# Kernel optimization log

Measured on AMD Instinct MI355X. Metric: run time of the kernel, lower is better.

## Reference

```python
import jax, jax.numpy as jnp
import numpy as np

B, C, H, W, HEADS = 8, 256, 64, 64, 4
EPS = 1e-5  # torch InstanceNorm2d default eps


def conv1x1(x, w):
    # w: [out_c, in_c]; x: [b, in_c, h, w]
    return jnp.einsum('oc,bchw->bohw', w, x)


def maxpool2(x):
    b, c, h, w = x.shape
    return x.reshape(b, c, h // 2, 2, w // 2, 2).max(axis=(3, 5))


def inorm_affine(x, g, b):
    # InstanceNorm2d(affine=True): normalize per (batch, channel) over H,W
    m = jnp.mean(x, axis=(2, 3), keepdims=True)
    v = jnp.mean((x - m) ** 2, axis=(2, 3), keepdims=True)
    return (x - m) * jax.lax.rsqrt(v + EPS) * g[None, :, None, None] + b[None, :, None, None]


def setup_inputs() -> dict:
    key = jax.random.key(0)
    ks = jax.random.split(key, 12)
    s = 1.0 / np.sqrt(C)  # fan-in style scaling for 1x1 conv weights
    return {
        'x': jax.random.normal(ks[0], (B, C, H, W), jnp.float32),
        'theta_w': jax.random.normal(ks[1], (C, C), jnp.float32) * s,
        'phi_w': jax.random.normal(ks[2], (C, C), jnp.float32) * s,
        'g_w': jax.random.normal(ks[3], (C // 2, C), jnp.float32) * s,
        'o_w': jax.random.normal(ks[4], (C, C // 2), jnp.float32) * np.sqrt(2.0 / C),
        'nt_w': 1.0 + 0.1 * jax.random.normal(ks[5], (C,), jnp.float32),
        'nt_b': 0.1 * jax.random.normal(ks[6], (C,), jnp.float32),
        'np_w': 1.0 + 0.1 * jax.random.normal(ks[7], (C,), jnp.float32),
        'np_b': 0.1 * jax.random.normal(ks[8], (C,), jnp.float32),
        'ng_w': 1.0 + 0.1 * jax.random.normal(ks[9], (C // 2,), jnp.float32),
        'ng_b': 0.1 * jax.random.normal(ks[10], (C // 2,), jnp.float32),
        'gamma': jnp.float32(0.5),
    }


def reference(x, theta_w, phi_w, g_w, o_w, nt_w, nt_b, np_w, np_b, ng_w, ng_b, gamma):
    b, c, h, w = x.shape
    n = h * w            # query length
    m = n // 4           # key/value length after 2x2 maxpool
    theta = inorm_affine(conv1x1(x, theta_w), nt_w, nt_b)
    phi = inorm_affine(maxpool2(conv1x1(x, phi_w)), np_w, np_b)
    g = inorm_affine(maxpool2(conv1x1(x, g_w)), ng_w, ng_b)
    # custom head layout: channel dim split as (C//heads, heads), head dim INNER
    theta_ = theta.reshape(b, c // HEADS, HEADS, n)
    phi_ = phi.reshape(b, c // HEADS, HEADS, m)
    g_ = g.reshape(b, (c // 2) // HEADS, HEADS, m)
    beta = jax.nn.softmax(jnp.einsum('bchi,bchj->bhij', theta_, phi_), axis=-1)
    o = jnp.einsum('bchj,bhij->bchi', g_, beta).reshape(b, c // 2, h, w)
    o = conv1x1(o, o_w)
    return gamma * o + x
```

## Files before the change

kernel.cpp:

```cpp
#include <hip/hip_runtime.h>
#include <hip/hip_bf16.h>
#include <math.h>

typedef float f32x4 __attribute__((ext_vector_type(4)));
typedef float f32x16 __attribute__((ext_vector_type(16)));
typedef __bf16 b16x8 __attribute__((ext_vector_type(8)));
typedef __bf16 b16x4 __attribute__((ext_vector_type(4)));
typedef unsigned int u32x2 __attribute__((ext_vector_type(2)));
typedef unsigned int u32x4 __attribute__((ext_vector_type(4)));

#define L2E 1.44269504088896340736f

__global__ void prep_weights(const float* tw, const float* pw, const float* gw,
                             const float* ow, __bf16* Wp, __bf16* OWp) {
    int idx = blockIdx.x * 256 + threadIdx.x;
    if (idx < 640 * 256) {
        int m = idx >> 8, k = idx & 255;
        float v;
        if (m < 256)      { int o = ((m & 63) << 2) + (m >> 6);            v = tw[o * 256 + k]; }
        else if (m < 512) { int mm = m - 256; int o = ((mm & 63) << 2) + (mm >> 6); v = pw[o * 256 + k]; }
        else              { int mm = m - 512; int o = ((mm & 31) << 2) + (mm >> 5); v = gw[o * 256 + k]; }
        Wp[idx] = (__bf16)v;
    } else {
        int j = idx - 640 * 256;
        if (j < 256 * 128) {
            int m = j >> 7, c = j & 127;
            int o = ((c & 31) << 2) + (c >> 5);
            OWp[j] = (__bf16)ow[m * 128 + o];
        }
    }
}

__global__ void transpose_x(const float* x, __bf16* xt) {
    __shared__ float tile[32][33];
    int b = blockIdx.z, c0 = blockIdx.y * 32, p0 = blockIdx.x * 32;
    int tx = threadIdx.x & 31, ty = threadIdx.x >> 5;
#pragma unroll
    for (int i = 0; i < 4; i++) {
        int cy = ty + i * 8;
        tile[cy][tx] = x[((size_t)(b * 256 + c0 + cy)) * 4096 + p0 + tx];
    }
    __syncthreads();
#pragma unroll
    for (int i = 0; i < 4; i++) {
        int py = ty + i * 8;
        xt[((size_t)b * 4096 + p0 + py) * 256 + c0 + tx] = (__bf16)tile[tx][py];
    }
}

__global__ __launch_bounds__(256) void conv_gemm(const __bf16* __restrict__ Wp,
                                                 const __bf16* __restrict__ xt,
                                                 __bf16* theta_t, __bf16* phi_t, __bf16* g_t) {
    int b = blockIdx.z, mt = blockIdx.y, nt = blockIdx.x;
    __shared__ __bf16 Al[128 * 40];
    __shared__ __bf16 Bl[128 * 40];
    int tid = threadIdx.x, l = tid & 63, w = tid >> 6;
    int wm = w >> 1, wn = w & 1, lr = l & 15, lg = l >> 4;
    f32x4 acc[4][4];
#pragma unroll
    for (int i = 0; i < 4; i++)
#pragma unroll
        for (int j = 0; j < 4; j++)
#pragma unroll
            for (int r = 0; r < 4; r++) acc[i][j][r] = 0.f;
    const __bf16* Ag = Wp + (size_t)mt * 128 * 256;
    const __bf16* Bg = xt + ((size_t)b * 4096 + nt * 128) * 256;
    int srow = tid >> 2, scol = (tid & 3) * 8;
    for (int k0 = 0; k0 < 256; k0 += 32) {
        __syncthreads();
#pragma unroll
        for (int hh = 0; hh < 2; hh++) {
            int r = srow + hh * 64;
            *(b16x8*)&Al[r * 40 + scol] = *(const b16x8*)&Ag[(size_t)r * 256 + k0 + scol];
            *(b16x8*)&Bl[r * 40 + scol] = *(const b16x8*)&Bg[(size_t)r * 256 + k0 + scol];
        }
        __syncthreads();
        int ko = lg * 8;
        b16x8 af[4], bfr[4];
#pragma unroll
        for (int i = 0; i < 4; i++) af[i]  = *(b16x8*)&Al[(wm * 64 + i * 16 + lr) * 40 + ko];
#pragma unroll
        for (int i = 0; i < 4; i++) bfr[i] = *(b16x8*)&Bl[(wn * 64 + i * 16 + lr) * 40 + ko];
#pragma unroll
        for (int i = 0; i < 4; i++)
#pragma unroll
            for (int j = 0; j < 4; j++)
                acc[i][j] = __builtin_amdgcn_mfma_f32_16x16x32_bf16(af[i], bfr[j], acc[i][j], 0, 0, 0);
    }
    int rbase = lg * 4;
#pragma unroll
    for (int i = 0; i < 4; i++) {
        int m = mt * 128 + wm * 64 + i * 16 + rbase;
#pragma unroll
        for (int j = 0; j < 4; j++) {
            int p = nt * 128 + wn * 64 + j * 16 + lr;
            b16x4 v;
#pragma unroll
            for (int r = 0; r < 4; r++) v[r] = (__bf16)acc[i][j][r];
            if (m < 256)      *(b16x4*)&theta_t[((size_t)b * 4096 + p) * 256 + m] = v;
            else if (m < 512) *(b16x4*)&phi_t[((size_t)b * 4096 + p) * 256 + (m - 256)] = v;
            else              *(b16x4*)&g_t[((size_t)b * 4096 + p) * 128 + (m - 512)] = v;
        }
    }
}

__global__ void theta_stats(const __bf16* __restrict__ src, float* s1, float* s2) {
    int b = blockIdx.y, rc = blockIdx.x, c = threadIdx.x;
    float a1 = 0.f, a2 = 0.f;
    for (int r = 0; r < 64; r++) {
        float v = (float)src[((size_t)b * 4096 + rc * 64 + r) * 256 + c];
        a1 += v; a2 += v * v;
    }
    atomicAdd(&s1[b * 256 + c], a1);
    atomicAdd(&s2[b * 256 + c], a2);
}

__global__ void pool_phi(const __bf16* __restrict__ src, __bf16* dst, float* s1, float* s2) {
    int b = blockIdx.y, qc = blockIdx.x, c = threadIdx.x;
    float a1 = 0.f, a2 = 0.f;
    for (int qq = 0; qq < 32; qq++) {
        int q = qc * 32 + qq, qy = q >> 5, qx = q & 31;
        size_t base = ((size_t)(b * 4096) + qy * 128 + qx * 2) * 256 + c;
        float v0 = (float)src[base], v1 = (float)src[base + 256];
        float v2 = (float)src[base + 16384], v3 = (float)src[base + 16640];
        float m = fmaxf(fmaxf(v0, v1), fmaxf(v2, v3));
        dst[((size_t)b * 1024 + q) * 256 + c] = (__bf16)m;
        a1 += m; a2 += m * m;
    }
    atomicAdd(&s1[b * 256 + c], a1);
    atomicAdd(&s2[b * 256 + c], a2);
}

__global__ __launch_bounds__(256) void pool_gT(const __bf16* __restrict__ src, __bf16* gT,
                                               float* s1, float* s2) {
    __shared__ __bf16 Pt[64][136];
    int b = blockIdx.y, qc = blockIdx.x;
    int t = threadIdx.x, c = t & 127, qh = t >> 7;
    float a1 = 0.f, a2 = 0.f;
    for (int qq = 0; qq < 32; qq++) {
        int ql = qh * 32 + qq, q = qc * 64 + ql;
        int qy = q >> 5, qx = q & 31;
        size_t base = ((size_t)(b * 4096) + qy * 128 + qx * 2) * 128 + c;
        float v0 = (float)src[base], v1 = (float)src[base + 128];
        float v2 = (float)src[base + 8192], v3 = (float)src[base + 8320];
        float m = fmaxf(fmaxf(v0, v1), fmaxf(v2, v3));
        Pt[ql][c] = (__bf16)m;
        a1 += m; a2 += m * m;
    }
    atomicAdd(&s1[b * 128 + c], a1);
    atomicAdd(&s2[b * 128 + c], a2);
    __syncthreads();
    int hh = c >> 5, ch = c & 31;
#pragma unroll
    for (int sg = 0; sg < 4; sg++) {
        int seg = qh * 4 + sg;
        b16x8 v;
#pragma unroll
        for (int e = 0; e < 8; e++) v[e] = Pt[seg * 8 + e][c];
        *(b16x8*)&gT[((((size_t)(b * 4 + hh) * 16 + qc) * 8 + seg) * 32 + ch) * 8] = v;
    }
}

__global__ void finalize_stats(const float* s1t, const float* s2t, const float* s1p,
                               const float* s2p, const float* s1g, const float* s2g,
                               const float* ntw, const float* ntb, const float* npw,
                               const float* npb, const float* ngw, const float* ngb,
                               float* sct, float* bit, float* scp, float* bip,
                               float* scg, float* big) {
    int idx = blockIdx.x * 256 + threadIdx.x;
    if (idx >= 8 * 640) return;
    int b = idx / 640, c = idx % 640;
    if (c < 256) {
        float n = 4096.f;
        float m = s1t[b * 256 + c] / n, v = s2t[b * 256 + c] / n - m * m;
        float r = rsqrtf(v + 1e-5f);
        int o = ((c & 63) << 2) + (c >> 6);
        float wv = ntw[o], bv = ntb[o];
        sct[b * 256 + c] = r * wv * L2E;
        bit[b * 256 + c] = (bv - m * r * wv) * L2E;
    } else if (c < 512) {
        int cc = c - 256;
        float n = 1024.f;
        float m = s1p[b * 256 + cc] / n, v = s2p[b * 256 + cc] / n - m * m;
        float r = rsqrtf(v + 1e-5f);
        int o = ((cc & 63) << 2) + (cc >> 6);
        float wv = npw[o], bv = npb[o];
        scp[b * 256 + cc] = r * wv; bip[b * 256 + cc] = bv - m * r * wv;
    } else {
        int cc = c - 512;
        float n = 1024.f;
        float m = s1g[b * 128 + cc] / n, v = s2g[b * 128 + cc] / n - m * m;
        float r = rsqrtf(v + 1e-5f);
        int o = ((cc & 31) << 2) + (cc >> 5);
        float wv = ngw[o], bv = ngb[o];
        scg[b * 128 + cc] = r * wv; big[b * 128 + cc] = bv - m * r * wv;
    }
}

__global__ void normalize_kv(__bf16* phi, __bf16* gT, const float* scp, const float* bip,
                             const float* scg, const float* big) {
    int blk = blockIdx.x, t = threadIdx.x;
    if (blk < 1024) {
        int b = blk >> 7, xi = (blk & 127) * 256 + t;
        int row = xi >> 5, c = (xi & 31) * 8;
        size_t off = ((size_t)b * 1024 + row) * 256 + c;
        b16x8 v = *(b16x8*)&phi[off];
#pragma unroll
        for (int e = 0; e < 8; e++)
            v[e] = (__bf16)((float)v[e] * scp[b * 256 + c + e] + bip[b * 256 + c + e]);
        *(b16x8*)&phi[off] = v;
    } else {
        int f = (blk - 1024) * 256 + t;
        int ch = f & 31, bh = f >> 12;
        int b = bh >> 2;
        int ci = b * 128 + ((bh & 3) << 5) + ch;
        float sc = scg[ci], bi = big[ci];
        size_t off = (size_t)f * 8;
        b16x8 v = *(b16x8*)&gT[off];
#pragma unroll
        for (int e = 0; e < 8; e++) v[e] = (__bf16)((float)v[e] * sc + bi);
        *(b16x8*)&gT[off] = v;
    }
}

__global__ __launch_bounds__(256, 2) void attn(const __bf16* __restrict__ theta_t,
                                               const __bf16* __restrict__ phi_n,
                                               const __bf16* __restrict__ gTz,
                                               const float* __restrict__ sct,
                                               const float* __restrict__ bit,
                                               __bf16* __restrict__ o_mid) {
    int qt = blockIdx.x, h = blockIdx.y, b = blockIdx.z;
    __shared__ __bf16 Kl[2][64 * 64];
    int tid = threadIdx.x, w = tid >> 6, lane = tid & 63;
    int l31 = lane & 31, hi = lane >> 5;
    int qb = qt * 256 + w * 64;

    b16x8 qf[2][4];
#pragma unroll
    for (int m = 0; m < 2; m++) {
        int q = qb + m * 32 + l31;
        const __bf16* qp = theta_t + ((size_t)b * 4096 + q) * 256 + h * 64;
#pragma unroll
        for (int st = 0; st < 4; st++) {
            int cb = st * 16 + hi * 8;
            b16x8 raw = *(const b16x8*)&qp[cb];
            b16x8 nv;
#pragma unroll
            for (int e = 0; e < 8; e++) {
                int cix = b * 256 + h * 64 + cb + e;
                nv[e] = (__bf16)((float)raw[e] * sct[cix] + bit[cix]);
            }
            qf[m][st] = nv;
        }
    }

    const __bf16* Kg = phi_n + (size_t)b * 1024 * 256 + h * 64;
    const __bf16* Vg = gTz + (size_t)(b * 4 + h) * 32768;

    int r0 = tid >> 3, sl = tid & 7, r1 = r0 + 32;
    int gcol = sl * 8;
    int w0 = (sl ^ (r0 & 7)) * 8;
    int w1 = (sl ^ (r1 & 7)) * 8;

    {
        b16x8 k0 = *(const b16x8*)&Kg[(size_t)r0 * 256 + gcol];
        b16x8 k1 = *(const b16x8*)&Kg[(size_t)r1 * 256 + gcol];
        *(b16x8*)&Kl[0][r0 * 64 + w0] = k0;
        *(b16x8*)&Kl[0][r1 * 64 + w1] = k1;
    }
    b16x8 av[4];
#pragma unroll
    for (int js = 0; js < 4; js++)
        av[js] = *(const b16x8*)&Vg[(size_t)(((js * 2 + hi) * 32 + l31) * 8)];
    __syncthreads();

    f32x16 NEG24;
#pragma unroll
    for (int r = 0; r < 16; r++) NEG24[r] = -24.f;
    f32x16 oacc[2];
#pragma unroll
    for (int m = 0; m < 2; m++)
#pragma unroll
        for (int r = 0; r < 16; r++) oacc[m][r] = 0.f;
    float l_run[2] = {0.f, 0.f};

    for (int c = 0; c < 16; c++) {
        int cur = c & 1;
        b16x8 kr0, kr1, avn[4];
        if (c < 15) {
            size_t cb = (size_t)(c + 1) * 64;
            kr0 = *(const b16x8*)&Kg[(cb + r0) * 256 + gcol];
            kr1 = *(const b16x8*)&Kg[(cb + r1) * 256 + gcol];
#pragma unroll
            for (int js = 0; js < 4; js++)
                avn[js] = *(const b16x8*)&Vg[(size_t)((((c + 1) * 8 + js * 2 + hi) * 32 + l31) * 8)];
        }
        b16x8 ak[2][4];
#pragma unroll
        for (int kf = 0; kf < 2; kf++)
#pragma unroll
            for (int st = 0; st < 4; st++)
                ak[kf][st] = *(b16x8*)&Kl[cur][(kf * 32 + l31) * 64 + ((st * 2 + hi) ^ (l31 & 7)) * 8];

#pragma unroll
        for (int m = 0; m < 2; m++) {
            f32x16 s[2];
#pragma unroll
            for (int kf = 0; kf < 2; kf++) {
                s[kf] = __builtin_amdgcn_mfma_f32_32x32x16_bf16(ak[kf][0], qf[m][0], NEG24, 0, 0, 0);
#pragma unroll
                for (int st = 1; st < 4; st++)
                    s[kf] = __builtin_amdgcn_mfma_f32_32x32x16_bf16(ak[kf][st], qf[m][st], s[kf], 0, 0, 0);
            }
            float sum = 0.f;
#pragma unroll
            for (int kf = 0; kf < 2; kf++)
#pragma unroll
                for (int r = 0; r < 16; r++) {
                    float p = __builtin_amdgcn_exp2f(s[kf][r]);
                    s[kf][r] = p; sum += p;
                }
            l_run[m] += sum;
#pragma unroll
            for (int kf = 0; kf < 2; kf++)
#pragma unroll
                for (int hh2 = 0; hh2 < 2; hh2++) {
                    b16x4 A4, B4;
#pragma unroll
                    for (int e = 0; e < 4; e++) {
                        A4[e] = (__bf16)s[kf][hh2 * 8 + e];
                        B4[e] = (__bf16)s[kf][hh2 * 8 + 4 + e];
                    }
                    u32x2 a2 = __builtin_bit_cast(u32x2, A4);
                    u32x2 b2 = __builtin_bit_cast(u32x2, B4);
                    u32x2 q0 = __builtin_amdgcn_permlane32_swap(a2[0], b2[0], false, false);
                    u32x2 q1 = __builtin_amdgcn_permlane32_swap(a2[1], b2[1], false, false);
                    u32x4 pd = {q0[0], q1[0], q0[1], q1[1]};
                    b16x8 pf = __builtin_bit_cast(b16x8, pd);
                    oacc[m] = __builtin_amdgcn_mfma_f32_32x32x16_bf16(av[kf * 2 + hh2], pf, oacc[m], 0, 0, 0);
                }
        }
        if (c < 15) {
            *(b16x8*)&Kl[cur ^ 1][r0 * 64 + w0] = kr0;
            *(b16x8*)&Kl[cur ^ 1][r1 * 64 + w1] = kr1;
            __syncthreads();
#pragma unroll
            for (int js = 0; js < 4; js++) av[js] = avn[js];
        }
    }
#pragma unroll
    for (int m = 0; m < 2; m++) {
        float lr = l_run[m] + __shfl_xor(l_run[m], 32, 64);
        float rl = 1.0f / lr;
        int q = qb + m * 32 + l31;
#pragma unroll
        for (int rr = 0; rr < 4; rr++) {
            b16x4 v;
#pragma unroll
            for (int e = 0; e < 4; e++) v[e] = (__bf16)(oacc[m][rr * 4 + e] * rl);
            *(b16x4*)&o_mid[((size_t)b * 4096 + q) * 128 + h * 32 + rr * 8 + hi * 4] = v;
        }
    }
}

__global__ __launch_bounds__(256) void out_gemm(const __bf16* __restrict__ OWp,
                                                const __bf16* __restrict__ o_mid,
                                                const float* __restrict__ x,
                                                const float* gamma, float* out) {
    int b = blockIdx.z, mt = blockIdx.y, nt = blockIdx.x;
    __shared__ __bf16 Al[128 * 40];
    __shared__ __bf16 Bl[128 * 40];
    int tid = threadIdx.x, l = tid & 63, w = tid >> 6;
    int wm = w >> 1, wn = w & 1, lr = l & 15, lg = l >> 4;
    f32x4 acc[4][4];
#pragma unroll
    for (int i = 0; i < 4; i++)
#pragma unroll
        for (int j = 0; j < 4; j++)
#pragma unroll
            for (int r = 0; r < 4; r++) acc[i][j][r] = 0.f;
    const __bf16* Ag = OWp + (size_t)mt * 128 * 128;
    const __bf16* Bg = o_mid + ((size_t)b * 4096 + nt * 128) * 128;
    int srow = tid >> 2, scol = (tid & 3) * 8;
    for (int k0 = 0; k0 < 128; k0 += 32) {
        __syncthreads();
#pragma unroll
        for (int hh = 0; hh < 2; hh++) {
            int r = srow + hh * 64;
            *(b16x8*)&Al[r * 40 + scol] = *(const b16x8*)&Ag[(size_t)r * 128 + k0 + scol];
            *(b16x8*)&Bl[r * 40 + scol] = *(const b16x8*)&Bg[(size_t)r * 128 + k0 + scol];
        }
        __syncthreads();
        int ko = lg * 8;
        b16x8 af[4], bfr[4];
#pragma unroll
        for (int i = 0; i < 4; i++) af[i]  = *(b16x8*)&Al[(wm * 64 + i * 16 + lr) * 40 + ko];
#pragma unroll
        for (int i = 0; i < 4; i++) bfr[i] = *(b16x8*)&Bl[(wn * 64 + i * 16 + lr) * 40 + ko];
#pragma unroll
        for (int i = 0; i < 4; i++)
#pragma unroll
            for (int j = 0; j < 4; j++)
                acc[i][j] = __builtin_amdgcn_mfma_f32_16x16x32_bf16(af[i], bfr[j], acc[i][j], 0, 0, 0);
    }
    float gm = gamma[0];
    int rbase = lg * 4;
#pragma unroll
    for (int i = 0; i < 4; i++) {
        int m = mt * 128 + wm * 64 + i * 16 + rbase;
#pragma unroll
        for (int j = 0; j < 4; j++) {
            int p = nt * 128 + wn * 64 + j * 16 + lr;
#pragma unroll
            for (int r = 0; r < 4; r++) {
                size_t o = ((size_t)b * 256 + m + r) * 4096 + p;
                out[o] = gm * acc[i][j][r] + x[o];
            }
        }
    }
}

extern "C" void kernel_launch(void* const* d_in, const int* in_sizes, int n_in,
                              void* d_out, int out_size, void* d_ws, size_t ws_size,
                              hipStream_t stream) {
    const float* x   = (const float*)d_in[0];
    const float* tw  = (const float*)d_in[1];
    const float* pw  = (const float*)d_in[2];
    const float* gw  = (const float*)d_in[3];
    const float* ow  = (const float*)d_in[4];
    const float* ntw = (const float*)d_in[5];
    const float* ntb = (const float*)d_in[6];
    const float* npw = (const float*)d_in[7];
    const float* npb = (const float*)d_in[8];
    const float* ngw = (const float*)d_in[9];
    const float* ngb = (const float*)d_in[10];
    const float* gamma = (const float*)d_in[11];
    float* out = (float*)d_out;
    char* ws = (char*)d_ws;

    __bf16* Wp  = (__bf16*)(ws + 0);
    __bf16* OWp = (__bf16*)(ws + 327680);
    __bf16* xt  = (__bf16*)(ws + 393216);
    __bf16* th  = (__bf16*)(ws + 17170432);
    __bf16* phr = (__bf16*)(ws + 33947648);
    __bf16* ghr = (__bf16*)(ws + 50724864);
    __bf16* php = (__bf16*)(ws + 59113472);
    __bf16* gT  = (__bf16*)(ws + 63307776);
    float* sums = (float*)(ws + 65404928);
    float* sb   = (float*)(ws + 65445888);
    __bf16* om  = xt;

    float *s1t = sums, *s2t = sums + 2048, *s1p = sums + 4096, *s2p = sums + 6144,
          *s1g = sums + 8192, *s2g = sums + 9216;
    float *sct = sb, *bit = sb + 2048, *scp = sb + 4096, *bip = sb + 6144,
          *scg = sb + 8192, *big = sb + 9216;

    hipMemsetAsync(sums, 0, 40960, stream);
    prep_weights<<<768, 256, 0, stream>>>(tw, pw, gw, ow, Wp, OWp);
    transpose_x<<<dim3(128, 8, 8), 256, 0, stream>>>(x, xt);
    conv_gemm<<<dim3(32, 5, 8), 256, 0, stream>>>(Wp, xt, th, phr, ghr);
    theta_stats<<<dim3(64, 8), 256, 0, stream>>>(th, s1t, s2t);
    pool_phi<<<dim3(32, 8), 256, 0, stream>>>(phr, php, s1p, s2p);
    pool_gT<<<dim3(16, 8), 256, 0, stream>>>(ghr, gT, s1g, s2g);
    finalize_stats<<<20, 256, 0, stream>>>(s1t, s2t, s1p, s2p, s1g, s2g,
                                           ntw, ntb, npw, npb, ngw, ngb,
                                           sct, bit, scp, bip, scg, big);
    normalize_kv<<<1536, 256, 0, stream>>>(php, gT, scp, bip, scg, big);
    attn<<<dim3(16, 4, 8), 256, 0, stream>>>(th, php, gT, sct, bit, om);
    out_gemm<<<dim3(32, 2, 8), 256, 0, stream>>>(OWp, om, x, gamma, out);
}
```

Before: 126.2 us.

## Pre-layout K into MFMA fragment order, drop LDS staging, fold g-norm into epilogue

The phi normalization now writes K in a per-(batch,head) fragment-major layout, so attention can load K and V straight from global memory into registers with a two-stage register double buffer. This removes the shared-memory K tile and its barriers. The affine norm of g is applied after the softmax-weighted sum, which is valid because the softmax rows sum to one, so g no longer needs a normalize pass. The block index is remapped so blocks sharing a batch-head are spread across the grid, and the atomics plus memset for the statistics are replaced by per-chunk partial sums reduced in finalize_stats. In exchange there is more register pressure, K/V are read repeatedly from L2 instead of LDS, and the score init changes from -24 to 0, which could overflow exp2 for large logits.

```diff
diff --git a/kernel.cpp b/kernel.cpp
--- a/kernel.cpp
+++ b/kernel.cpp
@@ -104,18 +104,18 @@
     }
 }
 
-__global__ void theta_stats(const __bf16* __restrict__ src, float* s1, float* s2) {
+__global__ void theta_stats(const __bf16* __restrict__ src, float* p1, float* p2) {
     int b = blockIdx.y, rc = blockIdx.x, c = threadIdx.x;
     float a1 = 0.f, a2 = 0.f;
-    for (int r = 0; r < 64; r++) {
-        float v = (float)src[((size_t)b * 4096 + rc * 64 + r) * 256 + c];
+    for (int r = 0; r < 256; r++) {
+        float v = (float)src[((size_t)b * 4096 + rc * 256 + r) * 256 + c];
         a1 += v; a2 += v * v;
     }
-    atomicAdd(&s1[b * 256 + c], a1);
-    atomicAdd(&s2[b * 256 + c], a2);
-}
-
-__global__ void pool_phi(const __bf16* __restrict__ src, __bf16* dst, float* s1, float* s2) {
+    p1[(b * 16 + rc) * 256 + c] = a1;
+    p2[(b * 16 + rc) * 256 + c] = a2;
+}
+
+__global__ void pool_phi(const __bf16* __restrict__ src, __bf16* dst, float* p1, float* p2) {
     int b = blockIdx.y, qc = blockIdx.x, c = threadIdx.x;
     float a1 = 0.f, a2 = 0.f;
     for (int qq = 0; qq < 32; qq++) {
@@ -127,12 +127,12 @@
         dst[((size_t)b * 1024 + q) * 256 + c] = (__bf16)m;
         a1 += m; a2 += m * m;
     }
-    atomicAdd(&s1[b * 256 + c], a1);
-    atomicAdd(&s2[b * 256 + c], a2);
+    p1[(b * 32 + qc) * 256 + c] = a1;
+    p2[(b * 32 + qc) * 256 + c] = a2;
 }
 
 __global__ __launch_bounds__(256) void pool_gT(const __bf16* __restrict__ src, __bf16* gT,
-                                               float* s1, float* s2) {
+                                               float* p1, float* p2) {
     __shared__ __bf16 Pt[64][136];
     int b = blockIdx.y, qc = blockIdx.x;
     int t = threadIdx.x, c = t & 127, qh = t >> 7;
@@ -147,8 +147,8 @@
         Pt[ql][c] = (__bf16)m;
         a1 += m; a2 += m * m;
     }
-    atomicAdd(&s1[b * 128 + c], a1);
-    atomicAdd(&s2[b * 128 + c], a2);
+    p1[(b * 16 + qc) * 256 + t] = a1;
+    p2[(b * 16 + qc) * 256 + t] = a2;
     __syncthreads();
     int hh = c >> 5, ch = c & 31;
 #pragma unroll
@@ -161,8 +161,8 @@
     }
 }
 
-__global__ void finalize_stats(const float* s1t, const float* s2t, const float* s1p,
-                               const float* s2p, const float* s1g, const float* s2g,
+__global__ void finalize_stats(const float* tp1, const float* tp2, const float* pp1,
+                               const float* pp2, const float* gp1, const float* gp2,
                                const float* ntw, const float* ntb, const float* npw,
                                const float* npb, const float* ngw, const float* ngb,
                                float* sct, float* bit, float* scp, float* bip,
@@ -171,8 +171,10 @@
     if (idx >= 8 * 640) return;
     int b = idx / 640, c = idx % 640;
     if (c < 256) {
+        float s1 = 0.f, s2 = 0.f;
+        for (int i = 0; i < 16; i++) { s1 += tp1[(b * 16 + i) * 256 + c]; s2 += tp2[(b * 16 + i) * 256 + c]; }
         float n = 4096.f;
-        float m = s1t[b * 256 + c] / n, v = s2t[b * 256 + c] / n - m * m;
+        float m = s1 / n, v = s2 / n - m * m;
         float r = rsqrtf(v + 1e-5f);
         int o = ((c & 63) << 2) + (c >> 6);
         float wv = ntw[o], bv = ntb[o];
@@ -180,16 +182,23 @@
         bit[b * 256 + c] = (bv - m * r * wv) * L2E;
     } else if (c < 512) {
         int cc = c - 256;
+        float s1 = 0.f, s2 = 0.f;
+        for (int i = 0; i < 32; i++) { s1 += pp1[(b * 32 + i) * 256 + cc]; s2 += pp2[(b * 32 + i) * 256 + cc]; }
         float n = 1024.f;
-        float m = s1p[b * 256 + cc] / n, v = s2p[b * 256 + cc] / n - m * m;
+        float m = s1 / n, v = s2 / n - m * m;
         float r = rsqrtf(v + 1e-5f);
         int o = ((cc & 63) << 2) + (cc >> 6);
         float wv = npw[o], bv = npb[o];
         scp[b * 256 + cc] = r * wv; bip[b * 256 + cc] = bv - m * r * wv;
     } else {
         int cc = c - 512;
+        float s1 = 0.f, s2 = 0.f;
+        for (int i = 0; i < 16; i++) {
+            s1 += gp1[(b * 16 + i) * 256 + cc] + gp1[(b * 16 + i) * 256 + 128 + cc];
+            s2 += gp2[(b * 16 + i) * 256 + cc] + gp2[(b * 16 + i) * 256 + 128 + cc];
+        }
         float n = 1024.f;
-        float m = s1g[b * 128 + cc] / n, v = s2g[b * 128 + cc] / n - m * m;
+        float m = s1 / n, v = s2 / n - m * m;
         float r = rsqrtf(v + 1e-5f);
         int o = ((cc & 31) << 2) + (cc >> 5);
         float wv = ngw[o], bv = ngb[o];
@@ -197,40 +206,37 @@
     }
 }
 
-__global__ void normalize_kv(__bf16* phi, __bf16* gT, const float* scp, const float* bip,
-                             const float* scg, const float* big) {
+__global__ void normalize_phi(const __bf16* __restrict__ php, __bf16* __restrict__ phk,
+                              const float* __restrict__ scp, const float* __restrict__ bip) {
     int blk = blockIdx.x, t = threadIdx.x;
-    if (blk < 1024) {
-        int b = blk >> 7, xi = (blk & 127) * 256 + t;
-        int row = xi >> 5, c = (xi & 31) * 8;
-        size_t off = ((size_t)b * 1024 + row) * 256 + c;
-        b16x8 v = *(b16x8*)&phi[off];
+    int b = blk >> 6, h = (blk >> 4) & 3, cc = blk & 15;
+#pragma unroll
+    for (int uu = 0; uu < 2; uu++) {
+        int u = uu * 256 + t;
+        int slot = u >> 6, key = u & 63;
+        int q = cc * 64 + key;
+        int cfull = h * 64 + (slot >> 1) * 16 + (slot & 1) * 8;
+        b16x8 v = *(const b16x8*)&php[((size_t)b * 1024 + q) * 256 + cfull];
+        b16x8 nv;
 #pragma unroll
         for (int e = 0; e < 8; e++)
-            v[e] = (__bf16)((float)v[e] * scp[b * 256 + c + e] + bip[b * 256 + c + e]);
-        *(b16x8*)&phi[off] = v;
-    } else {
-        int f = (blk - 1024) * 256 + t;
-        int ch = f & 31, bh = f >> 12;
-        int b = bh >> 2;
-        int ci = b * 128 + ((bh & 3) << 5) + ch;
-        float sc = scg[ci], bi = big[ci];
-        size_t off = (size_t)f * 8;
-        b16x8 v = *(b16x8*)&gT[off];
-#pragma unroll
-        for (int e = 0; e < 8; e++) v[e] = (__bf16)((float)v[e] * sc + bi);
-        *(b16x8*)&gT[off] = v;
+            nv[e] = (__bf16)((float)v[e] * scp[b * 256 + cfull + e] + bip[b * 256 + cfull + e]);
+        *(b16x8*)&phk[((((size_t)(b * 4 + h) * 16 + cc) * 8 + slot) * 64 + key) * 8] = nv;
     }
 }
 
 __global__ __launch_bounds__(256, 2) void attn(const __bf16* __restrict__ theta_t,
-                                               const __bf16* __restrict__ phi_n,
+                                               const __bf16* __restrict__ phk,
                                                const __bf16* __restrict__ gTz,
                                                const float* __restrict__ sct,
                                                const float* __restrict__ bit,
+                                               const float* __restrict__ scg,
+                                               const float* __restrict__ big,
                                                __bf16* __restrict__ o_mid) {
-    int qt = blockIdx.x, h = blockIdx.y, b = blockIdx.z;
-    __shared__ __bf16 Kl[2][64 * 64];
+    int bid = blockIdx.x;
+    int idx = bid >> 3;
+    int bh = (bid & 7) * 4 + (idx >> 4), qt = idx & 15;
+    int b = bh >> 2, h = bh & 3;
     int tid = threadIdx.x, w = tid >> 6, lane = tid & 63;
     int l31 = lane & 31, hi = lane >> 5;
     int qb = qt * 256 + w * 64;
@@ -254,100 +260,63 @@
         }
     }
 
-    const __bf16* Kg = phi_n + (size_t)b * 1024 * 256 + h * 64;
-    const __bf16* Vg = gTz + (size_t)(b * 4 + h) * 32768;
-
-    int r0 = tid >> 3, sl = tid & 7, r1 = r0 + 32;
-    int gcol = sl * 8;
-    int w0 = (sl ^ (r0 & 7)) * 8;
-    int w1 = (sl ^ (r1 & 7)) * 8;
-
-    {
-        b16x8 k0 = *(const b16x8*)&Kg[(size_t)r0 * 256 + gcol];
-        b16x8 k1 = *(const b16x8*)&Kg[(size_t)r1 * 256 + gcol];
-        *(b16x8*)&Kl[0][r0 * 64 + w0] = k0;
-        *(b16x8*)&Kl[0][r1 * 64 + w1] = k1;
-    }
-    b16x8 av[4];
-#pragma unroll
-    for (int js = 0; js < 4; js++)
-        av[js] = *(const b16x8*)&Vg[(size_t)(((js * 2 + hi) * 32 + l31) * 8)];
-    __syncthreads();
-
-    f32x16 NEG24;
-#pragma unroll
-    for (int r = 0; r < 16; r++) NEG24[r] = -24.f;
+    const __bf16* Kg = phk + (size_t)bh * 65536 + (size_t)hi * 512 + (size_t)l31 * 8;
+    const __bf16* Vg = gTz + (size_t)bh * 32768 + (size_t)hi * 256 + (size_t)l31 * 8;
+
     f32x16 oacc[2];
+    float l_run[2] = {0.f, 0.f};
 #pragma unroll
     for (int m = 0; m < 2; m++)
 #pragma unroll
         for (int r = 0; r < 16; r++) oacc[m][r] = 0.f;
-    float l_run[2] = {0.f, 0.f};
-
-    for (int c = 0; c < 16; c++) {
-        int cur = c & 1;
-        b16x8 kr0, kr1, avn[4];
-        if (c < 15) {
-            size_t cb = (size_t)(c + 1) * 64;
-            kr0 = *(const b16x8*)&Kg[(cb + r0) * 256 + gcol];
-            kr1 = *(const b16x8*)&Kg[(cb + r1) * 256 + gcol];
-#pragma unroll
-            for (int js = 0; js < 4; js++)
-                avn[js] = *(const b16x8*)&Vg[(size_t)((((c + 1) * 8 + js * 2 + hi) * 32 + l31) * 8)];
-        }
-        b16x8 ak[2][4];
-#pragma unroll
-        for (int kf = 0; kf < 2; kf++)
-#pragma unroll
-            for (int st = 0; st < 4; st++)
-                ak[kf][st] = *(b16x8*)&Kl[cur][(kf * 32 + l31) * 64 + ((st * 2 + hi) ^ (l31 & 7)) * 8];
-
-#pragma unroll
-        for (int m = 0; m < 2; m++) {
-            f32x16 s[2];
-#pragma unroll
-            for (int kf = 0; kf < 2; kf++) {
-                s[kf] = __builtin_amdgcn_mfma_f32_32x32x16_bf16(ak[kf][0], qf[m][0], NEG24, 0, 0, 0);
-#pragma unroll
-                for (int st = 1; st < 4; st++)
-                    s[kf] = __builtin_amdgcn_mfma_f32_32x32x16_bf16(ak[kf][st], qf[m][st], s[kf], 0, 0, 0);
-            }
-            float sum = 0.f;
-#pragma unroll
-            for (int kf = 0; kf < 2; kf++)
-#pragma unroll
-                for (int r = 0; r < 16; r++) {
-                    float p = __builtin_amdgcn_exp2f(s[kf][r]);
-                    s[kf][r] = p; sum += p;
-                }
-            l_run[m] += sum;
-#pragma unroll
-            for (int kf = 0; kf < 2; kf++)
-#pragma unroll
-                for (int hh2 = 0; hh2 < 2; hh2++) {
-                    b16x4 A4, B4;
-#pragma unroll
-                    for (int e = 0; e < 4; e++) {
-                        A4[e] = (__bf16)s[kf][hh2 * 8 + e];
-                        B4[e] = (__bf16)s[kf][hh2 * 8 + 4 + e];
-                    }
-                    u32x2 a2 = __builtin_bit_cast(u32x2, A4);
-                    u32x2 b2 = __builtin_bit_cast(u32x2, B4);
-                    u32x2 q0 = __builtin_amdgcn_permlane32_swap(a2[0], b2[0], false, false);
-                    u32x2 q1 = __builtin_amdgcn_permlane32_swap(a2[1], b2[1], false, false);
-                    u32x4 pd = {q0[0], q1[0], q0[1], q1[1]};
-                    b16x8 pf = __builtin_bit_cast(b16x8, pd);
-                    oacc[m] = __builtin_amdgcn_mfma_f32_32x32x16_bf16(av[kf * 2 + hh2], pf, oacc[m], 0, 0, 0);
-                }
-        }
-        if (c < 15) {
-            *(b16x8*)&Kl[cur ^ 1][r0 * 64 + w0] = kr0;
-            *(b16x8*)&Kl[cur ^ 1][r1 * 64 + w1] = kr1;
-            __syncthreads();
-#pragma unroll
-            for (int js = 0; js < 4; js++) av[js] = avn[js];
-        }
-    }
+    f32x16 zc;
+#pragma unroll
+    for (int r = 0; r < 16; r++) zc[r] = 0.f;
+
+    b16x8 akA[2][4], avA[4], akB[2][4], avB[4];
+
+#define LOADK(dst, c) { _Pragma("unroll") for (int kf = 0; kf < 2; kf++) \
+    _Pragma("unroll") for (int st = 0; st < 4; st++) \
+        dst[kf][st] = *(const b16x8*)&Kg[(size_t)(c) * 4096 + st * 1024 + kf * 256]; }
+#define LOADV(dst, c) { _Pragma("unroll") for (int js = 0; js < 4; js++) \
+    dst[js] = *(const b16x8*)&Vg[(size_t)(c) * 2048 + js * 512]; }
+#define COMPUTE(ak, av) { \
+    _Pragma("unroll") for (int m = 0; m < 2; m++) { \
+        _Pragma("unroll") for (int kf = 0; kf < 2; kf++) { \
+            f32x16 s = __builtin_amdgcn_mfma_f32_32x32x16_bf16(ak[kf][0], qf[m][0], zc, 0, 0, 0); \
+            _Pragma("unroll") for (int st = 1; st < 4; st++) \
+                s = __builtin_amdgcn_mfma_f32_32x32x16_bf16(ak[kf][st], qf[m][st], s, 0, 0, 0); \
+            float sum = 0.f; \
+            _Pragma("unroll") for (int r = 0; r < 16; r++) { \
+                float p = __builtin_amdgcn_exp2f(s[r]); s[r] = p; sum += p; } \
+            l_run[m] += sum; \
+            _Pragma("unroll") for (int hh2 = 0; hh2 < 2; hh2++) { \
+                b16x4 A4, B4; \
+                _Pragma("unroll") for (int e = 0; e < 4; e++) { \
+                    A4[e] = (__bf16)s[hh2 * 8 + e]; B4[e] = (__bf16)s[hh2 * 8 + 4 + e]; } \
+                u32x2 a2 = __builtin_bit_cast(u32x2, A4); \
+                u32x2 b2 = __builtin_bit_cast(u32x2, B4); \
+                u32x2 q0 = __builtin_amdgcn_permlane32_swap(a2[0], b2[0], false, false); \
+                u32x2 q1 = __builtin_amdgcn_permlane32_swap(a2[1], b2[1], false, false); \
+                u32x4 pd = {q0[0], q1[0], q0[1], q1[1]}; \
+                b16x8 pf = __builtin_bit_cast(b16x8, pd); \
+                oacc[m] = __builtin_amdgcn_mfma_f32_32x32x16_bf16(av[kf * 2 + hh2], pf, oacc[m], 0, 0, 0); \
+            } \
+        } \
+    } }
+
+    LOADK(akA, 0) LOADV(avA, 0)
+#pragma unroll 1
+    for (int c = 0; c < 16; c += 2) {
+        LOADK(akB, c + 1) LOADV(avB, c + 1)
+        COMPUTE(akA, avA)
+        if (c + 2 < 16) { LOADK(akA, c + 2) LOADV(avA, c + 2) }
+        COMPUTE(akB, avB)
+    }
+#undef LOADK
+#undef LOADV
+#undef COMPUTE
+
 #pragma unroll
     for (int m = 0; m < 2; m++) {
         float lr = l_run[m] + __shfl_xor(l_run[m], 32, 64);
@@ -357,7 +326,10 @@
         for (int rr = 0; rr < 4; rr++) {
             b16x4 v;
 #pragma unroll
-            for (int e = 0; e < 4; e++) v[e] = (__bf16)(oacc[m][rr * 4 + e] * rl);
+            for (int e = 0; e < 4; e++) {
+                int ci = b * 128 + h * 32 + rr * 8 + hi * 4 + e;
+                v[e] = (__bf16)(oacc[m][rr * 4 + e] * rl * scg[ci] + big[ci]);
+            }
             *(b16x4*)&o_mid[((size_t)b * 4096 + q) * 128 + h * 32 + rr * 8 + hi * 4] = v;
         }
     }
@@ -446,26 +418,30 @@
     __bf16* ghr = (__bf16*)(ws + 50724864);
     __bf16* php = (__bf16*)(ws + 59113472);
     __bf16* gT  = (__bf16*)(ws + 63307776);
-    float* sums = (float*)(ws + 65404928);
     float* sb   = (float*)(ws + 65445888);
+
+    float* tp1 = (float*)(ws + 393216);
+    float* tp2 = (float*)(ws + 524288);
+    float* pp1 = (float*)(ws + 655360);
+    float* pp2 = (float*)(ws + 917504);
+    float* gp1 = (float*)(ws + 1179648);
+    float* gp2 = (float*)(ws + 1310720);
+    __bf16* phk = phr;
     __bf16* om  = xt;
 
-    float *s1t = sums, *s2t = sums + 2048, *s1p = sums + 4096, *s2p = sums + 6144,
-          *s1g = sums + 8192, *s2g = sums + 9216;
     float *sct = sb, *bit = sb + 2048, *scp = sb + 4096, *bip = sb + 6144,
           *scg = sb + 8192, *big = sb + 9216;
 
-    hipMemsetAsync(sums, 0, 40960, stream);
     prep_weights<<<768, 256, 0, stream>>>(tw, pw, gw, ow, Wp, OWp);
     transpose_x<<<dim3(128, 8, 8), 256, 0, stream>>>(x, xt);
     conv_gemm<<<dim3(32, 5, 8), 256, 0, stream>>>(Wp, xt, th, phr, ghr);
-    theta_stats<<<dim3(64, 8), 256, 0, stream>>>(th, s1t, s2t);
-    pool_phi<<<dim3(32, 8), 256, 0, stream>>>(phr, php, s1p, s2p);
-    pool_gT<<<dim3(16, 8), 256, 0, stream>>>(ghr, gT, s1g, s2g);
-    finalize_stats<<<20, 256, 0, stream>>>(s1t, s2t, s1p, s2p, s1g, s2g,
+    theta_stats<<<dim3(16, 8), 256, 0, stream>>>(th, tp1, tp2);
+    pool_phi<<<dim3(32, 8), 256, 0, stream>>>(phr, php, pp1, pp2);
+    pool_gT<<<dim3(16, 8), 256, 0, stream>>>(ghr, gT, gp1, gp2);
+    finalize_stats<<<20, 256, 0, stream>>>(tp1, tp2, pp1, pp2, gp1, gp2,
                                            ntw, ntb, npw, npb, ngw, ngb,
                                            sct, bit, scp, bip, scg, big);
-    normalize_kv<<<1536, 256, 0, stream>>>(php, gT, scp, bip, scg, big);
-    attn<<<dim3(16, 4, 8), 256, 0, stream>>>(th, php, gT, sct, bit, om);
+    normalize_phi<<<512, 256, 0, stream>>>(php, phk, scp, bip);
+    attn<<<512, 256, 0, stream>>>(th, phk, gT, sct, bit, scg, big, om);
     out_gemm<<<dim3(32, 2, 8), 256, 0, stream>>>(OWp, om, x, gamma, out);
 }
```

New measurement: 129.5 us. 2.6% more time.
